# Kernel optimization log

Hardware: AMD Instinct MI355X
Metric: run time of the kernel (lower is better)

## Reference

```python
import jax, jax.numpy as jnp
import numpy as np


def setup_inputs() -> dict:
    key = jax.random.key(0)
    kx, kwi, kwh = jax.random.split(key, 3)
    B, T, F, H = 32, 2048, 512, 512
    x = jax.random.normal(kx, (B, T, F), dtype=jnp.float32)
    c0 = jnp.zeros((B, H), dtype=jnp.float32)
    h0 = jnp.zeros((B, H), dtype=jnp.float32)
    # Flax OptimizedLSTMCell: fused kernels, gates in (i, f, g, o) order.
    # Input projection has no bias; recurrent projection carries the bias.
    Wi = jax.random.normal(kwi, (F, 4 * H), dtype=jnp.float32) / np.sqrt(F)
    Wh = jax.random.normal(kwh, (H, 4 * H), dtype=jnp.float32) / np.sqrt(H)
    b = jnp.zeros((4 * H,), dtype=jnp.float32)
    return {"x": x, "c0": c0, "h0": h0, "Wi": Wi, "Wh": Wh, "b": b}


def reference(x, c0, h0, Wi, Wh, b):
    # x: [B, T, F]; scan over time (axis 1), matching nn.scan(in_axes=1, out_axes=1).
    def step(carry, xt):
        c, h = carry
        z = xt @ Wi + h @ Wh + b  # [B, 4H]
        i, f, g, o = jnp.split(z, 4, axis=-1)
        i = jax.nn.sigmoid(i)
        f = jax.nn.sigmoid(f)
        g = jnp.tanh(g)
        o = jax.nn.sigmoid(o)
        c_new = f * c + i * g
        h_new = o * jnp.tanh(c_new)
        return (c_new, h_new), h_new

    xs = jnp.swapaxes(x, 0, 1)  # [T, B, F]
    (c_fin, h_fin), ys = jax.lax.scan(step, (c0, h0), xs)
    ys = jnp.swapaxes(ys, 0, 1)  # [B, T, H]
    return (c_fin, h_fin), ys
```

## Files before the change

### kernel.cpp

```cpp
#include <hip/hip_runtime.h>
#include <hip/hip_bf16.h>

#define B_    32
#define T_    2048
#define F_    512
#define H_    512
#define G_    64
#define NCOL  32
#define WPITCH 520
#define SLOT  (B_ * H_)
#define DSL   64

typedef __attribute__((ext_vector_type(8))) short short8;
typedef __attribute__((ext_vector_type(4))) float floatx4;

static __device__ __forceinline__ short bf16s(float f) {
    return __builtin_bit_cast(short, __float2bfloat16(f));
}
__device__ __forceinline__ float sigmoidf_(float x) {
    return 1.0f / (1.0f + __expf(-x));
}

__global__ void prep_kernel(const float* __restrict__ x,
                            const float* __restrict__ h0,
                            unsigned short* __restrict__ xb,
                            unsigned short* __restrict__ h_slot_last,
                            int do_x)
{
    const int tid = threadIdx.x;
    if (blockIdx.x < 64) {
        const int idx = blockIdx.x * 256 + tid;
        h_slot_last[idx] = (unsigned short)bf16s(h0[idx]);
        return;
    }
    if (!do_x) return;
    const long long base = ((long long)(blockIdx.x - 64) * 256 + tid) * 8;
    const floatx4 a = *(const floatx4*)(x + base);
    const floatx4 b = *(const floatx4*)(x + base + 4);
    short8 s;
    s[0] = bf16s(a[0]); s[1] = bf16s(a[1]); s[2] = bf16s(a[2]); s[3] = bf16s(a[3]);
    s[4] = bf16s(b[0]); s[5] = bf16s(b[1]); s[6] = bf16s(b[2]); s[7] = bf16s(b[3]);
    *(short8*)(xb + base) = s;
}

template<bool XB>
__global__ __launch_bounds__(256, 1)
void lstm_loop(const float* __restrict__ x,
               const unsigned short* __restrict__ xb,
               const float* __restrict__ c0,
               const float* __restrict__ Wi,
               const float* __restrict__ Wh,
               const float* __restrict__ bias,
               float* __restrict__ out,
               unsigned short* __restrict__ hbuf,
               unsigned int* __restrict__ flags)
{
    __shared__ short wtI[NCOL][WPITCH];
    __shared__ short wtH[NCOL][WPITCH];
    __shared__ float zbuf[B_][NCOL + 1];
    __shared__ __align__(16) unsigned short h_lds[B_][8];

    const int tid = threadIdx.x;
    const int wg  = blockIdx.x;

    for (int idx = tid; idx < NCOL * F_; idx += 256) {
        const int j  = idx & (NCOL - 1);
        const int k  = idx >> 5;
        const int gi = j >> 3, hc = j & 7;
        const int gcol = gi * H_ + wg * 8 + hc;
        wtI[j][k] = bf16s(Wi[k * (4 * H_) + gcol]);
        wtH[j][k] = bf16s(Wh[k * (4 * H_) + gcol]);
    }

    const int gb    = tid >> 3;
    const int ghc   = tid & 7;
    const int hglob = wg * 8 + ghc;
    float c_val  = c0[gb * H_ + hglob];
    float h_last = 0.f;
    const float bi = bias[0 * H_ + hglob];
    const float bf = bias[1 * H_ + hglob];
    const float bg = bias[2 * H_ + hglob];
    const float bo = bias[3 * H_ + hglob];

    const int wid  = tid >> 6;
    const int lane = tid & 63;
    const int mt   = wid >> 1;
    const int nt   = wid & 1;
    const int ln   = lane & 15;
    const int lq   = lane >> 4;
    const int arow = mt * 16 + ln;

    float* ys = out + 2 * B_ * H_;

    __syncthreads();

    for (int t = 0; t < T_; ++t) {
        floatx4 accx = {0.f, 0.f, 0.f, 0.f};
        if (XB) {
            const unsigned short* xrow = xb + (arow * T_ + t) * F_;
            #pragma unroll
            for (int ks = 0; ks < 16; ++ks) {
                const int koff = ks * 32 + lq * 8;
                const short8 ax = *(const short8*)(xrow + koff);
                const short8 bx = *(const short8*)&wtI[nt * 16 + ln][koff];
                accx = __builtin_amdgcn_mfma_f32_16x16x32_bf16(ax, bx, accx, 0, 0, 0);
            }
        } else {
            const float* xrow = x + (arow * T_ + t) * F_;
            #pragma unroll
            for (int ks = 0; ks < 16; ++ks) {
                const int koff = ks * 32 + lq * 8;
                const floatx4 xa = *(const floatx4*)(xrow + koff);
                const floatx4 xc = *(const floatx4*)(xrow + koff + 4);
                short8 ax;
                ax[0] = bf16s(xa[0]); ax[1] = bf16s(xa[1]);
                ax[2] = bf16s(xa[2]); ax[3] = bf16s(xa[3]);
                ax[4] = bf16s(xc[0]); ax[5] = bf16s(xc[1]);
                ax[6] = bf16s(xc[2]); ax[7] = bf16s(xc[3]);
                const short8 bx = *(const short8*)&wtI[nt * 16 + ln][koff];
                accx = __builtin_amdgcn_mfma_f32_16x16x32_bf16(ax, bx, accx, 0, 0, 0);
            }
        }

        if (t > 0) {
            if (wid == 0) {
                int spins = 0;
                while (true) {
                    const unsigned f = __hip_atomic_load(&flags[lane], __ATOMIC_RELAXED,
                                                         __HIP_MEMORY_SCOPE_AGENT);
                    if (__all((int)(f >= (unsigned)t))) break;
                    if (++spins > (1 << 16)) break;
                }
            }
            __syncthreads();
            if ((t & (DSL - 1)) == 0)
                __builtin_amdgcn_fence(__ATOMIC_ACQUIRE, "agent");
        }

        const unsigned short* hrow = hbuf + ((t - 1) & (DSL - 1)) * SLOT + arow * H_;
        floatx4 acch = {0.f, 0.f, 0.f, 0.f};
        #pragma unroll
        for (int ks = 0; ks < 16; ++ks) {
            const int koff = ks * 32 + lq * 8;
            const short8 ah = *(const short8*)(hrow + koff);
            const short8 bh = *(const short8*)&wtH[nt * 16 + ln][koff];
            acch = __builtin_amdgcn_mfma_f32_16x16x32_bf16(ah, bh, acch, 0, 0, 0);
        }
        {
            const int zrow = mt * 16 + lq * 4;
            const int zcol = nt * 16 + ln;
            #pragma unroll
            for (int r = 0; r < 4; ++r)
                zbuf[zrow + r][zcol] = accx[r] + acch[r];
        }
        __syncthreads();

        {
            const float zi = zbuf[gb][ghc]       + bi;
            const float zf = zbuf[gb][8  + ghc]  + bf;
            const float zg = zbuf[gb][16 + ghc]  + bg;
            const float zo = zbuf[gb][24 + ghc]  + bo;
            const float ig = sigmoidf_(zi);
            const float fg = sigmoidf_(zf);
            const float gg = tanhf(zg);
            const float og = sigmoidf_(zo);
            c_val  = fg * c_val + ig * gg;
            h_last = og * tanhf(c_val);
            h_lds[gb][ghc] = (unsigned short)bf16s(h_last);
            ys[(gb * T_ + t) * H_ + hglob] = h_last;
        }
        __syncthreads();

        if (tid < 64) {
            const int row = tid >> 1, c4 = (tid & 1) * 4;
            const unsigned long long v = *(const unsigned long long*)&h_lds[row][c4];
            __hip_atomic_store((unsigned long long*)(hbuf + (t & (DSL - 1)) * SLOT
                                                     + row * H_ + wg * 8 + c4),
                               v, __ATOMIC_RELAXED, __HIP_MEMORY_SCOPE_AGENT);
        }
        __syncthreads();
        if (tid == 0)
            __hip_atomic_store(&flags[wg], (unsigned)(t + 1), __ATOMIC_RELAXED,
                               __HIP_MEMORY_SCOPE_AGENT);
    }

    out[gb * H_ + hglob]           = c_val;
    out[B_ * H_ + gb * H_ + hglob] = h_last;
}

extern "C" void kernel_launch(void* const* d_in, const int* in_sizes, int n_in,
                              void* d_out, int out_size, void* d_ws, size_t ws_size,
                              hipStream_t stream) {
    const float* x  = (const float*)d_in[0];
    const float* c0 = (const float*)d_in[1];
    const float* h0 = (const float*)d_in[2];
    const float* Wi = (const float*)d_in[3];
    const float* Wh = (const float*)d_in[4];
    const float* b  = (const float*)d_in[5];
    float* out = (float*)d_out;

    unsigned char* ws = (unsigned char*)d_ws;
    unsigned int*   flags = (unsigned int*)ws;
    unsigned short* hbuf  = (unsigned short*)(ws + 65536);
    unsigned short* xb    = (unsigned short*)(ws + 65536 + (size_t)DSL * SLOT * 2);

    const size_t need_xb = 65536 + (size_t)DSL * SLOT * 2 + (size_t)B_ * T_ * F_ * 2;
    const int use_xb = (ws_size >= need_xb) ? 1 : 0;

    hipMemsetAsync(ws, 0, 4096, stream);

    const int prep_blocks = 64 + (use_xb ? (B_ * T_ * F_ / 8 / 256) : 0);
    prep_kernel<<<prep_blocks, 256, 0, stream>>>(x, h0, xb, hbuf + (DSL - 1) * SLOT, use_xb);

    void* args[] = { &x, &xb, &c0, &Wi, &Wh, &b, &out, &hbuf, &flags };
    hipLaunchCooperativeKernel(use_xb ? (void*)lstm_loop<true> : (void*)lstm_loop<false>,
                               dim3(G_), dim3(256), args, 0, stream);
}
```

Measured before the change: 10.29 ms.

## Replicate LSTM recurrence per XCD team with local-cache h exchange

Launches 8 teams of 32 workgroups and assigns each team to one XCD using the hardware XCC ID. Each team computes the full recurrence redundantly, and only team 0 writes outputs. Each workgroup now owns 16 hidden units and splits K across waves. Hidden-state exchange and flags use non-coherent (sc0 only) global loads and stores kept inside the XCD's L2, which avoids cross-die coherence latency on every timestep. It falls back to agent-scope (sc1) accesses if the XCD placement is not uniform. The ring buffer is shrunk, and the work per step is 8x redundant.

```diff
diff --git a/kernel.cpp b/kernel.cpp
--- a/kernel.cpp
+++ b/kernel.cpp
@@ -5,11 +5,14 @@
 #define T_    2048
 #define F_    512
 #define H_    512
-#define G_    64
-#define NCOL  32
+#define NTEAM 8
+#define NROLE 32
+#define NCOLS 64
+#define HCW   16
 #define WPITCH 520
 #define SLOT  (B_ * H_)
-#define DSL   64
+#define DSL   8
+#define TSTR  (DSL * SLOT)
 
 typedef __attribute__((ext_vector_type(8))) short short8;
 typedef __attribute__((ext_vector_type(4))) float floatx4;
@@ -19,28 +22,203 @@
 }
 __device__ __forceinline__ float sigmoidf_(float x) {
     return 1.0f / (1.0f + __expf(-x));
+}
+
+template<bool A>
+__device__ __forceinline__ short8 ldg16(const unsigned short* p) {
+    short8 v;
+    if (A) asm volatile("global_load_dwordx4 %0, %1, off sc0 sc1" : "=v"(v) : "v"(p) : "memory");
+    else   asm volatile("global_load_dwordx4 %0, %1, off sc0"     : "=v"(v) : "v"(p) : "memory");
+    return v;
+}
+template<bool A>
+__device__ __forceinline__ void stg16(unsigned short* p, short8 v) {
+    if (A) asm volatile("global_store_dwordx4 %0, %1, off sc0 sc1" :: "v"(p), "v"(v) : "memory");
+    else   asm volatile("global_store_dwordx4 %0, %1, off sc0"     :: "v"(p), "v"(v) : "memory");
+}
+template<bool A>
+__device__ __forceinline__ unsigned ldg4(const unsigned int* p) {
+    unsigned v;
+    if (A) asm volatile("global_load_dword %0, %1, off sc0 sc1\ns_waitcnt vmcnt(0)" : "=v"(v) : "v"(p) : "memory");
+    else   asm volatile("global_load_dword %0, %1, off sc0\ns_waitcnt vmcnt(0)"     : "=v"(v) : "v"(p) : "memory");
+    return v;
+}
+template<bool A>
+__device__ __forceinline__ void stg4(unsigned int* p, unsigned v) {
+    if (A) asm volatile("global_store_dword %0, %1, off sc0 sc1" :: "v"(p), "v"(v) : "memory");
+    else   asm volatile("global_store_dword %0, %1, off sc0"     :: "v"(p), "v"(v) : "memory");
 }
 
 __global__ void prep_kernel(const float* __restrict__ x,
                             const float* __restrict__ h0,
                             unsigned short* __restrict__ xb,
-                            unsigned short* __restrict__ h_slot_last,
+                            unsigned short* __restrict__ hbuf,
                             int do_x)
 {
     const int tid = threadIdx.x;
-    if (blockIdx.x < 64) {
-        const int idx = blockIdx.x * 256 + tid;
-        h_slot_last[idx] = (unsigned short)bf16s(h0[idx]);
+    if (blockIdx.x < NTEAM * 64) {
+        const int team = blockIdx.x >> 6;
+        const int idx  = (blockIdx.x & 63) * 256 + tid;
+        hbuf[(size_t)team * TSTR + (DSL - 1) * SLOT + idx] = (unsigned short)bf16s(h0[idx]);
         return;
     }
     if (!do_x) return;
-    const long long base = ((long long)(blockIdx.x - 64) * 256 + tid) * 8;
+    const long long base = ((long long)(blockIdx.x - NTEAM * 64) * 256 + tid) * 8;
     const floatx4 a = *(const floatx4*)(x + base);
     const floatx4 b = *(const floatx4*)(x + base + 4);
     short8 s;
     s[0] = bf16s(a[0]); s[1] = bf16s(a[1]); s[2] = bf16s(a[2]); s[3] = bf16s(a[3]);
     s[4] = bf16s(b[0]); s[5] = bf16s(b[1]); s[6] = bf16s(b[2]); s[7] = bf16s(b[3]);
     *(short8*)(xb + base) = s;
+}
+
+template<bool AGENT, bool XB>
+__device__ __forceinline__ void lstm_core(
+    const float* __restrict__ x, const unsigned short* __restrict__ xb,
+    const float* __restrict__ c0, const float* __restrict__ bias,
+    float* __restrict__ out,
+    unsigned short* hbt, unsigned int* flg,
+    const int role, const int wys,
+    short (*wtI)[WPITCH], short (*wtH)[WPITCH],
+    float (*zb)[B_][NCOLS + 2],
+    unsigned short (*h_lds)[HCW])
+{
+    const int tid = threadIdx.x;
+
+    const int gb = tid >> 3, hc = tid & 7;
+    const int hg0 = role * HCW + hc, hg1 = hg0 + 8;
+    float cv0 = c0[gb * H_ + hg0];
+    float cv1 = c0[gb * H_ + hg1];
+    float hl0 = 0.f, hl1 = 0.f;
+    const float bi0 = bias[0*H_+hg0], bf0 = bias[1*H_+hg0], bg0 = bias[2*H_+hg0], bo0 = bias[3*H_+hg0];
+    const float bi1 = bias[0*H_+hg1], bf1 = bias[1*H_+hg1], bg1 = bias[2*H_+hg1], bo1 = bias[3*H_+hg1];
+
+    const int wid = tid >> 6, lane = tid & 63;
+    const int mt = wid & 1, kh = wid >> 1;
+    const int ln = lane & 15, lq = lane >> 4;
+    const int arow = mt * 16 + ln;
+    const int kbase = kh * 256;
+
+    float* ys = out + 2 * B_ * H_;
+
+    for (int t = 0; t < T_; ++t) {
+        floatx4 accx[4] = {{0.f,0.f,0.f,0.f},{0.f,0.f,0.f,0.f},{0.f,0.f,0.f,0.f},{0.f,0.f,0.f,0.f}};
+        if (XB) {
+            const unsigned short* xrow = xb + (size_t)(arow * T_ + t) * F_ + kbase;
+            #pragma unroll
+            for (int ks = 0; ks < 8; ++ks) {
+                const int ko = ks * 32 + lq * 8;
+                const short8 ax = *(const short8*)(xrow + ko);
+                #pragma unroll
+                for (int nt = 0; nt < 4; ++nt) {
+                    const short8 bx = *(const short8*)&wtI[nt * 16 + ln][kbase + ko];
+                    accx[nt] = __builtin_amdgcn_mfma_f32_16x16x32_bf16(ax, bx, accx[nt], 0, 0, 0);
+                }
+            }
+        } else {
+            const float* xrow = x + (size_t)(arow * T_ + t) * F_ + kbase;
+            #pragma unroll
+            for (int ks = 0; ks < 8; ++ks) {
+                const int ko = ks * 32 + lq * 8;
+                const floatx4 xa = *(const floatx4*)(xrow + ko);
+                const floatx4 xc = *(const floatx4*)(xrow + ko + 4);
+                short8 ax;
+                ax[0] = bf16s(xa[0]); ax[1] = bf16s(xa[1]); ax[2] = bf16s(xa[2]); ax[3] = bf16s(xa[3]);
+                ax[4] = bf16s(xc[0]); ax[5] = bf16s(xc[1]); ax[6] = bf16s(xc[2]); ax[7] = bf16s(xc[3]);
+                #pragma unroll
+                for (int nt = 0; nt < 4; ++nt) {
+                    const short8 bx = *(const short8*)&wtI[nt * 16 + ln][kbase + ko];
+                    accx[nt] = __builtin_amdgcn_mfma_f32_16x16x32_bf16(ax, bx, accx[nt], 0, 0, 0);
+                }
+            }
+        }
+
+        if (t > 0) {
+            if (wid == 0) {
+                int spins = 0;
+                while (true) {
+                    const unsigned f = ldg4<AGENT>(&flg[lane & (NROLE - 1)]);
+                    if (__all((int)(f >= (unsigned)t))) break;
+                    if (++spins > (1 << 20)) break;
+                }
+            }
+            __syncthreads();
+        }
+
+        const unsigned short* hrow = hbt + ((t - 1) & (DSL - 1)) * SLOT + arow * H_ + kbase;
+        short8 ah[8];
+        #pragma unroll
+        for (int ks = 0; ks < 8; ++ks)
+            ah[ks] = ldg16<AGENT>(hrow + ks * 32 + lq * 8);
+        asm volatile("s_waitcnt vmcnt(0)" ::: "memory");
+        __builtin_amdgcn_sched_barrier(0);
+
+        floatx4 acch[4] = {{0.f,0.f,0.f,0.f},{0.f,0.f,0.f,0.f},{0.f,0.f,0.f,0.f},{0.f,0.f,0.f,0.f}};
+        #pragma unroll
+        for (int ks = 0; ks < 8; ++ks) {
+            const int ko = kbase + ks * 32 + lq * 8;
+            #pragma unroll
+            for (int nt = 0; nt < 4; ++nt) {
+                const short8 bh = *(const short8*)&wtH[nt * 16 + ln][ko];
+                acch[nt] = __builtin_amdgcn_mfma_f32_16x16x32_bf16(ah[ks], bh, acch[nt], 0, 0, 0);
+            }
+        }
+        {
+            const int zrow = mt * 16 + lq * 4;
+            #pragma unroll
+            for (int nt = 0; nt < 4; ++nt) {
+                const int zcol = nt * 16 + ln;
+                #pragma unroll
+                for (int r = 0; r < 4; ++r)
+                    zb[kh][zrow + r][zcol] = accx[nt][r] + acch[nt][r];
+            }
+        }
+        __syncthreads();
+
+        {
+            const float zi0 = zb[0][gb][hc]      + zb[1][gb][hc]      + bi0;
+            const float zf0 = zb[0][gb][16 + hc] + zb[1][gb][16 + hc] + bf0;
+            const float zg0 = zb[0][gb][32 + hc] + zb[1][gb][32 + hc] + bg0;
+            const float zo0 = zb[0][gb][48 + hc] + zb[1][gb][48 + hc] + bo0;
+            const float i0 = sigmoidf_(zi0), f0 = sigmoidf_(zf0);
+            const float g0 = tanhf(zg0),     o0 = sigmoidf_(zo0);
+            cv0 = f0 * cv0 + i0 * g0;
+            hl0 = o0 * tanhf(cv0);
+            h_lds[gb][hc] = (unsigned short)bf16s(hl0);
+
+            const int h1 = hc + 8;
+            const float zi1 = zb[0][gb][h1]      + zb[1][gb][h1]      + bi1;
+            const float zf1 = zb[0][gb][16 + h1] + zb[1][gb][16 + h1] + bf1;
+            const float zg1 = zb[0][gb][32 + h1] + zb[1][gb][32 + h1] + bg1;
+            const float zo1 = zb[0][gb][48 + h1] + zb[1][gb][48 + h1] + bo1;
+            const float i1 = sigmoidf_(zi1), f1 = sigmoidf_(zf1);
+            const float g1 = tanhf(zg1),     o1 = sigmoidf_(zo1);
+            cv1 = f1 * cv1 + i1 * g1;
+            hl1 = o1 * tanhf(cv1);
+            h_lds[gb][h1] = (unsigned short)bf16s(hl1);
+
+            if (wys) {
+                ys[(size_t)(gb * T_ + t) * H_ + hg0] = hl0;
+                ys[(size_t)(gb * T_ + t) * H_ + hg1] = hl1;
+            }
+        }
+        __syncthreads();
+
+        if (tid < 64) {
+            const int row = tid >> 1, c8 = (tid & 1) * 8;
+            const short8 v = *(const short8*)&h_lds[row][c8];
+            stg16<AGENT>(hbt + (t & (DSL - 1)) * SLOT + row * H_ + role * HCW + c8, v);
+            asm volatile("s_waitcnt vmcnt(0)" ::: "memory");
+            if (tid == 0) stg4<AGENT>(&flg[role], (unsigned)(t + 1));
+        }
+    }
+
+    if (wys) {
+        out[gb * H_ + hg0] = cv0;
+        out[gb * H_ + hg1] = cv1;
+        out[B_ * H_ + gb * H_ + hg0] = hl0;
+        out[B_ * H_ + gb * H_ + hg1] = hl1;
+    }
 }
 
 template<bool XB>
@@ -53,139 +231,50 @@
                const float* __restrict__ bias,
                float* __restrict__ out,
                unsigned short* __restrict__ hbuf,
-               unsigned int* __restrict__ flags)
+               unsigned int* __restrict__ ctl)
 {
-    __shared__ short wtI[NCOL][WPITCH];
-    __shared__ short wtH[NCOL][WPITCH];
-    __shared__ float zbuf[B_][NCOL + 1];
-    __shared__ __align__(16) unsigned short h_lds[B_][8];
+    __shared__ short wtI[NCOLS][WPITCH];
+    __shared__ short wtH[NCOLS][WPITCH];
+    __shared__ float zb[2][B_][NCOLS + 2];
+    __shared__ __align__(16) unsigned short h_lds[B_][HCW];
+    __shared__ int s_role, s_team, s_mode, s_wys;
 
     const int tid = threadIdx.x;
-    const int wg  = blockIdx.x;
-
-    for (int idx = tid; idx < NCOL * F_; idx += 256) {
-        const int j  = idx & (NCOL - 1);
-        const int k  = idx >> 5;
-        const int gi = j >> 3, hc = j & 7;
-        const int gcol = gi * H_ + wg * 8 + hc;
+
+    if (tid == 0) {
+        int xcd;
+        asm volatile("s_getreg_b32 %0, hwreg(HW_REG_XCC_ID)" : "=s"(xcd));
+        xcd &= (NTEAM - 1);
+        const unsigned role  = __hip_atomic_fetch_add(&ctl[xcd], 1u, __ATOMIC_ACQ_REL, __HIP_MEMORY_SCOPE_AGENT);
+        const unsigned grank = __hip_atomic_fetch_add(&ctl[8],   1u, __ATOMIC_ACQ_REL, __HIP_MEMORY_SCOPE_AGENT);
+        while (__hip_atomic_load(&ctl[8], __ATOMIC_ACQUIRE, __HIP_MEMORY_SCOPE_AGENT)
+               < (unsigned)(NTEAM * NROLE)) {}
+        int ok = 1;
+        for (int i = 0; i < NTEAM; ++i)
+            ok &= (__hip_atomic_load(&ctl[i], __ATOMIC_ACQUIRE, __HIP_MEMORY_SCOPE_AGENT)
+                   == (unsigned)NROLE);
+        s_mode = ok;
+        s_team = ok ? xcd : 0;
+        s_role = ok ? (int)role : (int)(grank & (NROLE - 1));
+        s_wys  = ok ? (xcd == 0) : (grank < (unsigned)NROLE);
+    }
+    __syncthreads();
+    const int mode = s_mode, role = s_role, team = s_team, wys = s_wys;
+
+    for (int idx = tid; idx < NCOLS * F_; idx += 256) {
+        const int j = idx & (NCOLS - 1);
+        const int k = idx >> 6;
+        const int gcol = (j >> 4) * H_ + role * HCW + (j & 15);
         wtI[j][k] = bf16s(Wi[k * (4 * H_) + gcol]);
         wtH[j][k] = bf16s(Wh[k * (4 * H_) + gcol]);
     }
-
-    const int gb    = tid >> 3;
-    const int ghc   = tid & 7;
-    const int hglob = wg * 8 + ghc;
-    float c_val  = c0[gb * H_ + hglob];
-    float h_last = 0.f;
-    const float bi = bias[0 * H_ + hglob];
-    const float bf = bias[1 * H_ + hglob];
-    const float bg = bias[2 * H_ + hglob];
-    const float bo = bias[3 * H_ + hglob];
-
-    const int wid  = tid >> 6;
-    const int lane = tid & 63;
-    const int mt   = wid >> 1;
-    const int nt   = wid & 1;
-    const int ln   = lane & 15;
-    const int lq   = lane >> 4;
-    const int arow = mt * 16 + ln;
-
-    float* ys = out + 2 * B_ * H_;
-
     __syncthreads();
 
-    for (int t = 0; t < T_; ++t) {
-        floatx4 accx = {0.f, 0.f, 0.f, 0.f};
-        if (XB) {
-            const unsigned short* xrow = xb + (arow * T_ + t) * F_;
-            #pragma unroll
-            for (int ks = 0; ks < 16; ++ks) {
-                const int koff = ks * 32 + lq * 8;
-                const short8 ax = *(const short8*)(xrow + koff);
-                const short8 bx = *(const short8*)&wtI[nt * 16 + ln][koff];
-                accx = __builtin_amdgcn_mfma_f32_16x16x32_bf16(ax, bx, accx, 0, 0, 0);
-            }
-        } else {
-            const float* xrow = x + (arow * T_ + t) * F_;
-            #pragma unroll
-            for (int ks = 0; ks < 16; ++ks) {
-                const int koff = ks * 32 + lq * 8;
-                const floatx4 xa = *(const floatx4*)(xrow + koff);
-                const floatx4 xc = *(const floatx4*)(xrow + koff + 4);
-                short8 ax;
-                ax[0] = bf16s(xa[0]); ax[1] = bf16s(xa[1]);
-                ax[2] = bf16s(xa[2]); ax[3] = bf16s(xa[3]);
-                ax[4] = bf16s(xc[0]); ax[5] = bf16s(xc[1]);
-                ax[6] = bf16s(xc[2]); ax[7] = bf16s(xc[3]);
-                const short8 bx = *(const short8*)&wtI[nt * 16 + ln][koff];
-                accx = __builtin_amdgcn_mfma_f32_16x16x32_bf16(ax, bx, accx, 0, 0, 0);
-            }
-        }
-
-        if (t > 0) {
-            if (wid == 0) {
-                int spins = 0;
-                while (true) {
-                    const unsigned f = __hip_atomic_load(&flags[lane], __ATOMIC_RELAXED,
-                                                         __HIP_MEMORY_SCOPE_AGENT);
-                    if (__all((int)(f >= (unsigned)t))) break;
-                    if (++spins > (1 << 16)) break;
-                }
-            }
-            __syncthreads();
-            if ((t & (DSL - 1)) == 0)
-                __builtin_amdgcn_fence(__ATOMIC_ACQUIRE, "agent");
-        }
-
-        const unsigned short* hrow = hbuf + ((t - 1) & (DSL - 1)) * SLOT + arow * H_;
-        floatx4 acch = {0.f, 0.f, 0.f, 0.f};
-        #pragma unroll
-        for (int ks = 0; ks < 16; ++ks) {
-            const int koff = ks * 32 + lq * 8;
-            const short8 ah = *(const short8*)(hrow + koff);
-            const short8 bh = *(const short8*)&wtH[nt * 16 + ln][koff];
-            acch = __builtin_amdgcn_mfma_f32_16x16x32_bf16(ah, bh, acch, 0, 0, 0);
-        }
-        {
-            const int zrow = mt * 16 + lq * 4;
-            const int zcol = nt * 16 + ln;
-            #pragma unroll
-            for (int r = 0; r < 4; ++r)
-                zbuf[zrow + r][zcol] = accx[r] + acch[r];
-        }
-        __syncthreads();
-
-        {
-            const float zi = zbuf[gb][ghc]       + bi;
-            const float zf = zbuf[gb][8  + ghc]  + bf;
-            const float zg = zbuf[gb][16 + ghc]  + bg;
-            const float zo = zbuf[gb][24 + ghc]  + bo;
-            const float ig = sigmoidf_(zi);
-            const float fg = sigmoidf_(zf);
-            const float gg = tanhf(zg);
-            const float og = sigmoidf_(zo);
-            c_val  = fg * c_val + ig * gg;
-            h_last = og * tanhf(c_val);
-            h_lds[gb][ghc] = (unsigned short)bf16s(h_last);
-            ys[(gb * T_ + t) * H_ + hglob] = h_last;
-        }
-        __syncthreads();
-
-        if (tid < 64) {
-            const int row = tid >> 1, c4 = (tid & 1) * 4;
-            const unsigned long long v = *(const unsigned long long*)&h_lds[row][c4];
-            __hip_atomic_store((unsigned long long*)(hbuf + (t & (DSL - 1)) * SLOT
-                                                     + row * H_ + wg * 8 + c4),
-                               v, __ATOMIC_RELAXED, __HIP_MEMORY_SCOPE_AGENT);
-        }
-        __syncthreads();
-        if (tid == 0)
-            __hip_atomic_store(&flags[wg], (unsigned)(t + 1), __ATOMIC_RELAXED,
-                               __HIP_MEMORY_SCOPE_AGENT);
-    }
-
-    out[gb * H_ + hglob]           = c_val;
-    out[B_ * H_ + gb * H_ + hglob] = h_last;
+    unsigned short* hbt = hbuf + (size_t)team * TSTR;
+    unsigned int*   flg = ctl + 256 + team * NROLE;
+
+    if (mode) lstm_core<false, XB>(x, xb, c0, bias, out, hbt, flg, role, wys, wtI, wtH, zb, h_lds);
+    else      lstm_core<true , XB>(x, xb, c0, bias, out, hbt, flg, role, wys, wtI, wtH, zb, h_lds);
 }
 
 extern "C" void kernel_launch(void* const* d_in, const int* in_sizes, int n_in,
@@ -200,19 +289,19 @@
     float* out = (float*)d_out;
 
     unsigned char* ws = (unsigned char*)d_ws;
-    unsigned int*   flags = (unsigned int*)ws;
-    unsigned short* hbuf  = (unsigned short*)(ws + 65536);
-    unsigned short* xb    = (unsigned short*)(ws + 65536 + (size_t)DSL * SLOT * 2);
-
-    const size_t need_xb = 65536 + (size_t)DSL * SLOT * 2 + (size_t)B_ * T_ * F_ * 2;
+    unsigned int*   ctl  = (unsigned int*)ws;
+    unsigned short* hbuf = (unsigned short*)(ws + 65536);
+    unsigned short* xb   = (unsigned short*)(ws + 65536 + (size_t)NTEAM * TSTR * 2);
+
+    const size_t need_xb = 65536 + (size_t)NTEAM * TSTR * 2 + (size_t)B_ * T_ * F_ * 2;
     const int use_xb = (ws_size >= need_xb) ? 1 : 0;
 
     hipMemsetAsync(ws, 0, 4096, stream);
 
-    const int prep_blocks = 64 + (use_xb ? (B_ * T_ * F_ / 8 / 256) : 0);
-    prep_kernel<<<prep_blocks, 256, 0, stream>>>(x, h0, xb, hbuf + (DSL - 1) * SLOT, use_xb);
-
-    void* args[] = { &x, &xb, &c0, &Wi, &Wh, &b, &out, &hbuf, &flags };
+    const int prep_blocks = NTEAM * 64 + (use_xb ? (B_ * T_ * F_ / 8 / 256) : 0);
+    prep_kernel<<<prep_blocks, 256, 0, stream>>>(x, h0, xb, hbuf, use_xb);
+
+    void* args[] = { &x, &xb, &c0, &Wi, &Wh, &b, &out, &hbuf, &ctl };
     hipLaunchCooperativeKernel(use_xb ? (void*)lstm_loop<true> : (void*)lstm_loop<false>,
-                               dim3(G_), dim3(256), args, 0, stream);
-}
+                               dim3(NTEAM * NROLE), dim3(256), args, 0, stream);
+}
```

After: 9.669 ms. 1.06x faster.
